# Kernel optimization log

Measured on AMD Instinct MI355X. Metric: run time of the kernel, lower is better.

The kernel has to match this reference:

```python
import jax, jax.numpy as jnp
import numpy as np

V, E, HS, HD = 32000, 64, 128, 128
S, T = 128, 48


def gru_cell(x, h, Wih, Whh, bih, bhh):
    # torch nn.GRU cell: gates stacked as [r, z, n]
    gi = x @ Wih.T + bih
    gh = h @ Whh.T + bhh
    ir, iz, inn = jnp.split(gi, 3, axis=-1)
    hr, hz, hn = jnp.split(gh, 3, axis=-1)
    r = jax.nn.sigmoid(ir + hr)
    z = jax.nn.sigmoid(iz + hz)
    n = jnp.tanh(inn + r * hn)
    return (1.0 - z) * n + z * h


def setup_inputs() -> dict:
    key = jax.random.key(0)
    ks = jax.random.split(key, 16)
    sc = 0.05
    inp = {
        'document': jax.random.randint(ks[0], (S, T), 0, V, dtype=jnp.int64),
        'enc_emb': jax.random.normal(ks[1], (V, E), jnp.float32) * sc,
        'enc_Wih': jax.random.normal(ks[2], (3 * HS, E), jnp.float32) * sc,
        'enc_Whh': jax.random.normal(ks[3], (3 * HS, HS), jnp.float32) * sc,
        'enc_bih': jax.random.normal(ks[4], (3 * HS,), jnp.float32) * sc,
        'enc_bhh': jax.random.normal(ks[5], (3 * HS,), jnp.float32) * sc,
        'doc_Wih': jax.random.normal(ks[6], (3 * HD, HS), jnp.float32) * sc,
        'doc_Whh': jax.random.normal(ks[7], (3 * HD, HD), jnp.float32) * sc,
        'doc_bih': jax.random.normal(ks[8], (3 * HD,), jnp.float32) * sc,
        'doc_bhh': jax.random.normal(ks[9], (3 * HD,), jnp.float32) * sc,
        'dec_emb': jax.random.normal(ks[10], (V, E), jnp.float32) * sc,
        'dec_Wih': jax.random.normal(ks[11], (3 * HS, E + HD), jnp.float32) * sc,
        'dec_Whh': jax.random.normal(ks[12], (3 * HS, HS), jnp.float32) * sc,
        'dec_bih': jax.random.normal(ks[13], (3 * HS,), jnp.float32) * sc,
        'dec_bhh': jax.random.normal(ks[14], (3 * HS,), jnp.float32) * sc,
        'fc_W': jax.random.normal(ks[15], (V, HS), jnp.float32) * sc,
        'fc_b': jnp.zeros((V,), jnp.float32),
    }
    return inp


def reference(document, enc_emb, enc_Wih, enc_Whh, enc_bih, enc_bhh,
              doc_Wih, doc_Whh, doc_bih, doc_bhh,
              dec_emb, dec_Wih, dec_Whh, dec_bih, dec_bhh, fc_W, fc_b):
    s, t = document.shape
    # --- sentence encoder: GRU over tokens, batch = sentences ---
    x = enc_emb[document]                       # [S, T, E]
    def enc_step(h, xt):
        return gru_cell(xt, h, enc_Wih, enc_Whh, enc_bih, enc_bhh), None
    h0 = jnp.zeros((s, HS), enc_emb.dtype)
    sent_vec, _ = jax.lax.scan(enc_step, h0, jnp.swapaxes(x, 0, 1))  # [S, HS]
    # --- document encoder: GRU over sentence vectors, batch = 1 ---
    def doc_step(h, sv):
        return gru_cell(sv[None, :], h, doc_Wih, doc_Whh, doc_bih, doc_bhh), None
    hd0 = jnp.zeros((1, HD), enc_emb.dtype)
    doc_h, _ = jax.lax.scan(doc_step, hd0, sent_vec)
    doc_vec = doc_h[0]                          # [HD]
    # --- teacher-forced decoder, vectorized over sentences ---
    dec_in = dec_emb[document[:, :-1]]          # [S, T-1, E]
    ctx = jnp.broadcast_to(doc_vec, (s, t - 1, HD))
    xs = jnp.swapaxes(jnp.concatenate([dec_in, ctx], axis=-1), 0, 1)  # [T-1, S, E+HD]
    def dec_step(h, xt):
        h2 = gru_cell(xt, h, dec_Wih, dec_Whh, dec_bih, dec_bhh)
        logits = h2 @ fc_W.T + fc_b
        return h2, logits
    _, logits = jax.lax.scan(dec_step, sent_vec, xs)  # [T-1, S, V]
    targets = document[:, 1:].T                 # [T-1, S]
    logp = jax.nn.log_softmax(logits, axis=-1)
    ll = jnp.take_along_axis(logp, targets[..., None], axis=-1)[..., 0]
    # per-sentence mean over steps, then mean over sentences == global mean
    return -jnp.mean(ll)
```

## Files before the change

### kernel.cpp

```cpp
#include <hip/hip_runtime.h>

typedef unsigned short ushort_t;
typedef short bf16x8 __attribute__((ext_vector_type(8)));
typedef float f32x4 __attribute__((ext_vector_type(4)));
typedef unsigned int u32x4 __attribute__((ext_vector_type(4)));
typedef _Float16 half2t __attribute__((ext_vector_type(2)));

#define LOG2E 1.4426950408889634f
#define LN2   0.6931471805599453f

__device__ __forceinline__ float bf2f(ushort_t u) {
    union { unsigned int i; float f; } v; v.i = ((unsigned int)u) << 16; return v.f;
}
__device__ __forceinline__ ushort_t f2bf(float f) {
    union { float f; unsigned int i; } v; v.f = f;
    unsigned int u = v.i;
    unsigned int r = (u + 0x7FFFu + ((u >> 16) & 1u)) >> 16;
    return (ushort_t)r;
}
__device__ __forceinline__ float hsum4(f32x4 v) { return (v[0] + v[1]) + (v[2] + v[3]); }
__device__ __forceinline__ float frcp(float x) { return __builtin_amdgcn_rcpf(x); }
__device__ __forceinline__ float fsig(float x) { return frcp(1.f + __expf(-x)); }
__device__ __forceinline__ float ftanh(float x) { return 1.f - 2.f * frcp(1.f + __expf(2.f * x)); }
__device__ __forceinline__ int hpad(int e) { return e + ((e >> 4) << 2); }
__device__ __forceinline__ float dot2(unsigned int w, unsigned int h, float acc) {
    union { unsigned int u; half2t h2; } a, b;
    a.u = w; b.u = h;
    return __builtin_amdgcn_fdot2(a.h2, b.h2, acc, false);
}
__device__ __forceinline__ float dpp_xor1_add(float x) {
    int m = __builtin_amdgcn_update_dpp(0, __builtin_bit_cast(int, x), 0xB1, 0xF, 0xF, true);
    return x + __builtin_bit_cast(float, m);
}
__device__ __forceinline__ float dpp_xor2_add(float x) {
    int m = __builtin_amdgcn_update_dpp(0, __builtin_bit_cast(int, x), 0x4E, 0xF, 0xF, true);
    return x + __builtin_bit_cast(float, m);
}
__device__ __forceinline__ ushort_t f2h(float f) {
    union { _Float16 h; ushort_t s; } c; c.h = (_Float16)f; return c.s;
}

__global__ void k_prep(const float* __restrict__ encWih, const float* __restrict__ encWhh,
                       const float* __restrict__ decWhh, const float* __restrict__ docWhh,
                       ushort_t* __restrict__ wencih, ushort_t* __restrict__ wenchh,
                       ushort_t* __restrict__ wdechh, ushort_t* __restrict__ wdoc) {
    int i = blockIdx.x * blockDim.x + threadIdx.x;
    const float* src; ushort_t* dst; int off;
    if (i < 6144)       { src = encWih; dst = wencih; off = i; }
    else if (i < 18432) { src = encWhh; dst = wenchh; off = i - 6144; }
    else if (i < 30720) { src = decWhh; dst = wdechh; off = i - 18432; }
    else if (i < 43008) { src = docWhh; dst = wdoc;   off = i - 30720; }
    else return;
    f32x4 v = ((const f32x4*)src)[off];
    union { ushort_t u[4]; unsigned long long q; } p;
    p.u[0] = f2h(v[0]); p.u[1] = f2h(v[1]); p.u[2] = f2h(v[2]); p.u[3] = f2h(v[3]);
    ((unsigned long long*)dst)[off] = p.q;
}

__global__ __launch_bounds__(768, 1) void k_encoder(
    const int* __restrict__ doc, const float* __restrict__ emb,
    const ushort_t* __restrict__ wih16, const ushort_t* __restrict__ whh16,
    const float* __restrict__ bih, const float* __restrict__ bhh,
    float* __restrict__ sent) {
    int s = blockIdx.x, t = threadIdx.x;
    int half = t & 1, j = t >> 1;
    __shared__ unsigned int xpk[32], hpk_[64];
    __shared__ float gi[384], gh[384];
    __shared__ int toks[48];
    u32x4 wi[4], wh[8];
    const ushort_t* pih = wih16 + j * 64 + half * 32;
    const ushort_t* phh = whh16 + j * 128 + half * 64;
#pragma unroll
    for (int k = 0; k < 4; k++) wi[k] = *(const u32x4*)(pih + k * 8);
#pragma unroll
    for (int k = 0; k < 8; k++) wh[k] = *(const u32x4*)(phh + k * 8);
    float bi = bih[j], bh = bhh[j];
    if (t < 48) toks[t] = doc[s * 48 + t];
    if (t < 64) hpk_[t] = 0u;
    __syncthreads();
    if (t < 64) ((ushort_t*)xpk)[t] = f2h(emb[(size_t)toks[0] * 64 + t]);
    float h_own = 0.f;
    __syncthreads();
    const unsigned int* xb = xpk + half * 16;
    const unsigned int* hb = hpk_ + half * 32;
    for (int tt = 0; tt < 48; tt++) {
        float xnext = (t < 64 && tt + 1 < 48) ? emb[(size_t)toks[tt + 1] * 64 + t] : 0.f;
        float a0 = 0.f, a1 = 0.f, b0 = 0.f, b1 = 0.f;
#pragma unroll
        for (int k = 0; k < 4; k++) {
            u32x4 xv = *(const u32x4*)(xb + k * 4);
            a0 = dot2(wi[k][0], xv[0], a0); a1 = dot2(wi[k][1], xv[1], a1);
            a0 = dot2(wi[k][2], xv[2], a0); a1 = dot2(wi[k][3], xv[3], a1);
        }
#pragma unroll
        for (int k = 0; k < 8; k++) {
            u32x4 hv = *(const u32x4*)(hb + k * 4);
            b0 = dot2(wh[k][0], hv[0], b0); b1 = dot2(wh[k][1], hv[1], b1);
            b0 = dot2(wh[k][2], hv[2], b0); b1 = dot2(wh[k][3], hv[3], b1);
        }
        float a = dpp_xor1_add(a0 + a1), b = dpp_xor1_add(b0 + b1);
        if (half == 0) { gi[j] = a + bi; gh[j] = b + bh; }
        __syncthreads();
        if (t < 128) {
            float r = fsig(gi[t] + gh[t]);
            float z = fsig(gi[t + 128] + gh[t + 128]);
            float n = ftanh(gi[t + 256] + r * gh[t + 256]);
            h_own = (1.f - z) * n + z * h_own;
            ((ushort_t*)hpk_)[t] = f2h(h_own);
        }
        if (t < 64 && tt + 1 < 48) ((ushort_t*)xpk)[t] = f2h(xnext);
        __syncthreads();
    }
    if (t < 128) sent[s * 128 + t] = h_own;
}

__global__ void k_doc_gi(const float* __restrict__ sv, const float* __restrict__ Wih,
                         const float* __restrict__ bih, float* __restrict__ gidoc) {
    int i = blockIdx.x, j = threadIdx.x;
    __shared__ f32x4 v4[32];
    if (j < 128) ((float*)v4)[j] = sv[i * 128 + j];
    __syncthreads();
    f32x4 a0 = {0,0,0,0}, a1 = {0,0,0,0};
#pragma unroll
    for (int k = 0; k < 32; k += 2) {
        a0 += *(const f32x4*)(Wih + j * 128 + k * 4) * v4[k];
        a1 += *(const f32x4*)(Wih + j * 128 + (k + 1) * 4) * v4[k + 1];
    }
    gidoc[i * 384 + j] = bih[j] + hsum4(a0 + a1);
}

__global__ __launch_bounds__(512, 1) __attribute__((amdgpu_waves_per_eu(1, 2)))
void k_mid(
    const float* __restrict__ gidoc, const ushort_t* __restrict__ wdoc,
    const float* __restrict__ dbhh, float* __restrict__ dvec,
    const int* __restrict__ doc, const float* __restrict__ demb,
    const float* __restrict__ dWih, float* __restrict__ gidec,
    const float* __restrict__ fcW, ushort_t* __restrict__ fcWb,
    const float* __restrict__ fcb, float* __restrict__ fcbs) {
    int bid = blockIdx.x, t = threadIdx.x;

    if (bid == 0) {
        int q = t & 3, e = t >> 2;
        __shared__ unsigned int hpk[2][64];
        u32x4 wr4[4], wz4[4], wn4[4];
        const ushort_t* wbase = wdoc + e * 128 + q * 32;
#pragma unroll
        for (int k = 0; k < 4; k++) {
            wr4[k] = *(const u32x4*)(wbase + k * 8);
            wz4[k] = *(const u32x4*)(wbase + 128 * 128 + k * 8);
            wn4[k] = *(const u32x4*)(wbase + 256 * 128 + k * 8);
        }
        float biasr = dbhh[e], biasz = dbhh[128 + e], biasn = dbhh[256 + e];
        float cr = gidoc[e], cz = gidoc[128 + e], cn = gidoc[256 + e];
        if (t < 64) hpk[0][t] = 0u;
        float he = 0.f;
        __syncthreads();
        for (int i = 0; i < 128; i++) {
            float nr = 0.f, nz = 0.f, nn = 0.f;
            if (i + 1 < 128) {
                const float* g = gidoc + (i + 1) * 384;
                nr = g[e]; nz = g[128 + e]; nn = g[256 + e];
            }
            const unsigned int* hp = &hpk[i & 1][q * 16];
            u32x4 hv[4];
            hv[0] = *(const u32x4*)(hp);
            hv[1] = *(const u32x4*)(hp + 4);
            hv[2] = *(const u32x4*)(hp + 8);
            hv[3] = *(const u32x4*)(hp + 12);
            float ra0 = 0.f, ra1 = 0.f, za0 = 0.f, za1 = 0.f, na0 = 0.f, na1 = 0.f;
#pragma unroll
            for (int k = 0; k < 4; k++) {
                u32x4 h4 = hv[k];
                ra0 = dot2(wr4[k][0], h4[0], ra0); ra1 = dot2(wr4[k][1], h4[1], ra1);
                ra0 = dot2(wr4[k][2], h4[2], ra0); ra1 = dot2(wr4[k][3], h4[3], ra1);
                za0 = dot2(wz4[k][0], h4[0], za0); za1 = dot2(wz4[k][1], h4[1], za1);
                za0 = dot2(wz4[k][2], h4[2], za0); za1 = dot2(wz4[k][3], h4[3], za1);
                na0 = dot2(wn4[k][0], h4[0], na0); na1 = dot2(wn4[k][1], h4[1], na1);
                na0 = dot2(wn4[k][2], h4[2], na0); na1 = dot2(wn4[k][3], h4[3], na1);
            }
            float rp = ra0 + ra1, zp = za0 + za1, np = na0 + na1;
            rp = dpp_xor2_add(dpp_xor1_add(rp));
            zp = dpp_xor2_add(dpp_xor1_add(zp));
            np = dpp_xor2_add(dpp_xor1_add(np));
            float r = fsig(cr + rp + biasr);
            float z = fsig(cz + zp + biasz);
            float n = ftanh(cn + r * (np + biasn));
            he = (1.f - z) * n + z * he;
            if (q == 0) ((ushort_t*)&hpk[(i & 1) ^ 1][0])[e] = f2h(he);
            __syncthreads();
            cr = nr; cz = nz; cn = nn;
        }
        if (q == 0) dvec[e] = he;
        return;
    }

    if (bid <= 128) {
        int s = bid - 1;
        __shared__ float xs[80];
        __shared__ int toks[48];
        if (t < 47) toks[t] = doc[s * 48 + t];
        __syncthreads();
        if (t < 64) xs[hpad(t)] = demb[(size_t)toks[0] * 64 + t];
        __syncthreads();
        f32x4 wih[16];
        if (t < 384) {
#pragma unroll
            for (int k = 0; k < 16; k++) wih[k] = *(const f32x4*)(dWih + t * 192 + k * 4);
        }
        for (int tt = 0; tt < 47; tt++) {
            float xnext = (t < 64 && tt + 1 < 47) ? demb[(size_t)toks[tt + 1] * 64 + t] : 0.f;
            if (t < 384) {
                f32x4 a0 = {0,0,0,0}, a1 = {0,0,0,0};
#pragma unroll
                for (int k = 0; k < 16; k += 2) {
                    a0 += wih[k] * (*(const f32x4*)(xs + k * 4 + (k >> 2) * 4));
                    a1 += wih[k + 1] * (*(const f32x4*)(xs + (k + 1) * 4 + ((k + 1) >> 2) * 4));
                }
                gidec[(tt * 128 + s) * 384 + t] = hsum4(a0 + a1);
            }
            __syncthreads();
            if (t < 64 && tt + 1 < 47) xs[hpad(t)] = xnext;
            __syncthreads();
        }
        return;
    }

    int i = (bid - 129) * 512 + t;
    if (i < 1024000) {
        f32x4 v = ((const f32x4*)fcW)[i];
        union { ushort_t u[4]; unsigned long long qq; } p;
        p.u[0] = f2bf(v[0] * LOG2E); p.u[1] = f2bf(v[1] * LOG2E);
        p.u[2] = f2bf(v[2] * LOG2E); p.u[3] = f2bf(v[3] * LOG2E);
        ((unsigned long long*)fcWb)[i] = p.qq;
    } else if (i < 1024000 + 8000) {
        int k = i - 1024000;
        f32x4 b = ((const f32x4*)fcb)[k];
        ((f32x4*)fcbs)[k] = b * LOG2E;
    }
}

__global__ void k_gctx(const float* __restrict__ Wih, const float* __restrict__ bih,
                       const float* __restrict__ dvec, float* __restrict__ gctx) {
    int j = threadIdx.x;
    __shared__ f32x4 v4[32];
    if (j < 128) ((float*)v4)[j] = dvec[j];
    __syncthreads();
    f32x4 a0 = {0,0,0,0}, a1 = {0,0,0,0};
#pragma unroll
    for (int k = 0; k < 32; k += 2) {
        a0 += *(const f32x4*)(Wih + j * 192 + 64 + k * 4) * v4[k];
        a1 += *(const f32x4*)(Wih + j * 192 + 64 + (k + 1) * 4) * v4[k + 1];
    }
    gctx[j] = bih[j] + hsum4(a0 + a1);
}

__global__ __launch_bounds__(768, 1) void k_dec_seq(
    const float* __restrict__ gidec, const ushort_t* __restrict__ whh16,
    const float* __restrict__ bhh, const float* __restrict__ sent,
    const float* __restrict__ gctx, ushort_t* __restrict__ h2b) {
    int s = blockIdx.x, t = threadIdx.x, half = t & 1, j = t >> 1;
    __shared__ unsigned int hpk_[64];
    __shared__ float gi[384], gh[384];
    u32x4 wh[8];
    const ushort_t* phh = whh16 + j * 128 + half * 64;
#pragma unroll
    for (int k = 0; k < 8; k++) wh[k] = *(const u32x4*)(phh + k * 8);
    float bh = bhh[j];
    float g_me = gctx[j];
    float h_own = 0.f;
    if (t < 128) { h_own = sent[s * 128 + t]; ((ushort_t*)hpk_)[t] = f2h(h_own); }
    float gval = (half == 0) ? (gidec[s * 384 + j] + g_me) : 0.f;
    __syncthreads();
    const unsigned int* hb = hpk_ + half * 32;
    for (int i = 0; i < 47; i++) {
        float gnext = (half == 0 && i + 1 < 47) ? (gidec[((i + 1) * 128 + s) * 384 + j] + g_me) : 0.f;
        float b0 = 0.f, b1 = 0.f;
#pragma unroll
        for (int k = 0; k < 8; k++) {
            u32x4 hv = *(const u32x4*)(hb + k * 4);
            b0 = dot2(wh[k][0], hv[0], b0); b1 = dot2(wh[k][1], hv[1], b1);
            b0 = dot2(wh[k][2], hv[2], b0); b1 = dot2(wh[k][3], hv[3], b1);
        }
        float b = dpp_xor1_add(b0 + b1);
        if (half == 0) { gh[j] = b + bh; gi[j] = gval; }
        __syncthreads();
        if (t < 128) {
            float r = fsig(gi[t] + gh[t]);
            float z = fsig(gi[t + 128] + gh[t + 128]);
            float n = ftanh(gi[t + 256] + r * gh[t + 256]);
            h_own = (1.f - z) * n + z * h_own;
            ((ushort_t*)hpk_)[t] = f2h(h_own);
            h2b[(i * 128 + s) * 128 + t] = f2bf(h_own);
        }
        __syncthreads();
        gval = gnext;
    }
}

__global__ void k_tl(const int* __restrict__ doc, const ushort_t* __restrict__ h2b,
                     const ushort_t* __restrict__ wb, const float* __restrict__ fcb,
                     float* __restrict__ tl) {
    int r = blockIdx.x * 4 + (threadIdx.x >> 6);
    int lane = threadIdx.x & 63;
    int s = r & 127, t = r >> 7;
    int tok = doc[s * 48 + t + 1];
    const ushort_t* hp = h2b + r * 128;
    const ushort_t* wp = wb + tok * 128;
    float acc = bf2f(hp[lane]) * bf2f(wp[lane]) + bf2f(hp[lane + 64]) * bf2f(wp[lane + 64]);
#pragma unroll
    for (int m = 32; m >= 1; m >>= 1) acc += __shfl_xor(acc, m);
    if (lane == 0) tl[r] = acc * LN2 + fcb[tok];
}

#define LSE_VC 10
#define LSE_NC 3200
#define LSE_NPAIR 25
__global__ __launch_bounds__(512, 2) void k_lse(
    const ushort_t* __restrict__ h2b, const ushort_t* __restrict__ wb,
    const float* __restrict__ fcbs, float* __restrict__ parts) {
    int rb = blockIdx.x / LSE_VC;
    int vc = blockIdx.x % LSE_VC;
    int t = threadIdx.x;
    int wave = t >> 6, lane = t & 63;
    int rg = wave >> 1, cg = wave & 1;
    int q = lane >> 4, l15 = lane & 15;

    __shared__ __align__(16) char ldsB[65536];

    int row0 = rb * 128 + rg * 32;
    bf16x8 a[2][4];
    const ushort_t* ap = h2b + (size_t)(row0 + l15) * 128 + q * 8;
#pragma unroll
    for (int m = 0; m < 2; m++)
#pragma unroll
        for (int c = 0; c < 4; c++) a[m][c] = *(const bf16x8*)(ap + m * 2048 + c * 32);

    const char* wbB = (const char*)wb;
    int so = ((t >> 4) << 8) + (((t & 15) ^ ((t >> 4) & 15)) << 4);
    char* dst1 = ldsB + wave * 1024;

#define LSE_STAGE(buf, cb) do { \
    const char* g_ = wbB + (size_t)(cb) * 256 + so; \
    char* d_ = dst1 + (buf) * 16384; \
    __builtin_amdgcn_global_load_lds((const __attribute__((address_space(1))) unsigned int*)(g_), \
                                     (__attribute__((address_space(3))) unsigned int*)(d_), 16, 0, 0); \
    __builtin_amdgcn_global_load_lds((const __attribute__((address_space(1))) unsigned int*)(g_ + 8192), \
                                     (__attribute__((address_space(3))) unsigned int*)(d_ + 8192), 16, 0, 0); \
} while (0)

    int ra[2][4];
#pragma unroll
    for (int c2 = 0; c2 < 2; c2++)
#pragma unroll
        for (int c = 0; c < 4; c++)
            ra[c2][c] = (cg * 32 + c2 * 16 + l15) * 256 + (((q + 4 * c) ^ l15) << 4);

    int cb0 = vc * LSE_NC;
    f32x4 se[2] = {{0,0,0,0},{0,0,0,0}};

    LSE_STAGE(0, cb0);
    LSE_STAGE(1, cb0 + 64);
    __syncthreads();
    int cur = 0;
    for (int it = 0; it < LSE_NPAIR; ++it) {
        if (it + 1 < LSE_NPAIR) {
            LSE_STAGE(2 * (cur ^ 1),     cb0 + (2 * it + 2) * 64);
            LSE_STAGE(2 * (cur ^ 1) + 1, cb0 + (2 * it + 3) * 64);
        }
        int colg = cb0 + 2 * it * 64 + cg * 32 + l15;
        float bA0 = fcbs[colg],      bA1 = fcbs[colg + 16];
        float bB0 = fcbs[colg + 64], bB1 = fcbs[colg + 80];
#pragma unroll
        for (int half = 0; half < 2; half++) {
            const char* bb = ldsB + (size_t)(2 * cur + half) * 16384;
            float bs0 = half ? bB0 : bA0;
            float bs1 = half ? bB1 : bA1;
            f32x4 acc[2][2] = {{{0,0,0,0},{0,0,0,0}},{{0,0,0,0},{0,0,0,0}}};
#pragma unroll
            for (int c = 0; c < 4; c++) {
                bf16x8 b0 = *(const bf16x8*)(bb + ra[0][c]);
                bf16x8 b1 = *(const bf16x8*)(bb + ra[1][c]);
                acc[0][0] = __builtin_amdgcn_mfma_f32_16x16x32_bf16(a[0][c], b0, acc[0][0], 0, 0, 0);
                acc[1][0] = __builtin_amdgcn_mfma_f32_16x16x32_bf16(a[1][c], b0, acc[1][0], 0, 0, 0);
                acc[0][1] = __builtin_amdgcn_mfma_f32_16x16x32_bf16(a[0][c], b1, acc[0][1], 0, 0, 0);
                acc[1][1] = __builtin_amdgcn_mfma_f32_16x16x32_bf16(a[1][c], b1, acc[1][1], 0, 0, 0);
            }
#pragma unroll
            for (int m = 0; m < 2; m++) {
#pragma unroll
                for (int r = 0; r < 4; r++)
                    se[m][r] += __builtin_amdgcn_exp2f(acc[m][0][r] + bs0)
                              + __builtin_amdgcn_exp2f(acc[m][1][r] + bs1);
            }
        }
        __syncthreads();
        cur ^= 1;
    }

#pragma unroll
    for (int m = 0; m < 2; m++) {
        f32x4 v = se[m];
#pragma unroll
        for (int d = 1; d < 16; d <<= 1) {
            v[0] += __shfl_xor(v[0], d);
            v[1] += __shfl_xor(v[1], d);
            v[2] += __shfl_xor(v[2], d);
            v[3] += __shfl_xor(v[3], d);
        }
        if (l15 == 0) {
            float* p = parts + (size_t)(vc * 2 + cg) * 6016 + row0 + m * 16 + q * 4;
            p[0] = v[0]; p[1] = v[1]; p[2] = v[2]; p[3] = v[3];
        }
    }
}

__global__ void k_final1(const float* __restrict__ parts, const float* __restrict__ tl,
                         float* __restrict__ rowloss) {
    int r = blockIdx.x * 128 + threadIdx.x;
    float tot = 0.f;
#pragma unroll 4
    for (int c = 0; c < 20; c++) tot += parts[(size_t)c * 6016 + r];
    rowloss[r] = logf(tot) - tl[r];
}

__global__ void k_final2(const float* __restrict__ rowloss, float* __restrict__ out) {
    __shared__ float red[512];
    int tid = threadIdx.x;
    float acc = 0.f;
    for (int r = tid; r < 6016; r += 512) acc += rowloss[r];
    red[tid] = acc;
    __syncthreads();
    for (int s = 256; s > 0; s >>= 1) {
        if (tid < s) red[tid] += red[tid + s];
        __syncthreads();
    }
    if (tid == 0) out[0] = red[0] / 6016.f;
}

extern "C" void kernel_launch(void* const* d_in, const int* in_sizes, int n_in,
                              void* d_out, int out_size, void* d_ws, size_t ws_size,
                              hipStream_t stream) {
    const int* doc = (const int*)d_in[0];
    const float* enc_emb = (const float*)d_in[1];
    const float* enc_Wih = (const float*)d_in[2];
    const float* enc_Whh = (const float*)d_in[3];
    const float* enc_bih = (const float*)d_in[4];
    const float* enc_bhh = (const float*)d_in[5];
    const float* doc_Wih = (const float*)d_in[6];
    const float* doc_Whh = (const float*)d_in[7];
    const float* doc_bih = (const float*)d_in[8];
    const float* doc_bhh = (const float*)d_in[9];
    const float* dec_emb = (const float*)d_in[10];
    const float* dec_Wih = (const float*)d_in[11];
    const float* dec_Whh = (const float*)d_in[12];
    const float* dec_bih = (const float*)d_in[13];
    const float* dec_bhh = (const float*)d_in[14];
    const float* fc_W = (const float*)d_in[15];
    const float* fc_b = (const float*)d_in[16];

    char* ws = (char*)d_ws;
    ushort_t* fcWb   = (ushort_t*)(ws + 0);
    float* sent      = (float*)(ws + 8192000);
    float* dvec      = (float*)(ws + 8257536);
    float* gidoc     = (float*)(ws + 8258048);
    float* gidec     = (float*)(ws + 8456192);
    ushort_t* h2b    = (ushort_t*)(ws + 17696768);
    float* tl        = (float*)(ws + 19236864);
    float* parts     = (float*)(ws + 19260928);
    float* rowloss   = (float*)(ws + 19742208);
    ushort_t* wdoc   = (ushort_t*)(ws + 19766272);
    float* fcbs      = (float*)(ws + 19864576);
    float* gctx      = (float*)(ws + 19992576);
    ushort_t* wencih = (ushort_t*)(ws + 19994112);
    ushort_t* wenchh = (ushort_t*)(ws + 20043264);
    ushort_t* wdechh = (ushort_t*)(ws + 20141568);
    float* out = (float*)d_out;

    k_prep<<<168, 256, 0, stream>>>(enc_Wih, enc_Whh, dec_Whh, doc_Whh,
                                    wencih, wenchh, wdechh, wdoc);
    k_encoder<<<128, 768, 0, stream>>>(doc, enc_emb, wencih, wenchh, enc_bih, enc_bhh, sent);
    k_doc_gi<<<128, 384, 0, stream>>>(sent, doc_Wih, doc_bih, gidoc);
    k_mid<<<1 + 128 + 2016, 512, 0, stream>>>(gidoc, wdoc, doc_bhh, dvec,
                                              doc, dec_emb, dec_Wih, gidec,
                                              fc_W, fcWb, fc_b, fcbs);
    k_gctx<<<1, 384, 0, stream>>>(dec_Wih, dec_bih, dvec, gctx);
    k_dec_seq<<<128, 768, 0, stream>>>(gidec, wdechh, dec_bhh, sent, gctx, h2b);
    k_tl<<<1504, 256, 0, stream>>>(doc, h2b, fcWb, fc_b, tl);
    k_lse<<<47 * LSE_VC, 512, 0, stream>>>(h2b, fcWb, fcbs, parts);
    k_final1<<<47, 128, 0, stream>>>(parts, tl, rowloss);
    k_final2<<<1, 512, 0, stream>>>(rowloss, out);
}
```

Baseline: 231.1 us.

## Fold gctx into decoder kernel and split LSE vocab into finer chunks

```diff
diff --git a/kernel.cpp b/kernel.cpp
--- a/kernel.cpp
+++ b/kernel.cpp
@@ -239,38 +239,37 @@
     }
 }
 
-__global__ void k_gctx(const float* __restrict__ Wih, const float* __restrict__ bih,
-                       const float* __restrict__ dvec, float* __restrict__ gctx) {
-    int j = threadIdx.x;
-    __shared__ f32x4 v4[32];
-    if (j < 128) ((float*)v4)[j] = dvec[j];
-    __syncthreads();
-    f32x4 a0 = {0,0,0,0}, a1 = {0,0,0,0};
-#pragma unroll
-    for (int k = 0; k < 32; k += 2) {
-        a0 += *(const f32x4*)(Wih + j * 192 + 64 + k * 4) * v4[k];
-        a1 += *(const f32x4*)(Wih + j * 192 + 64 + (k + 1) * 4) * v4[k + 1];
-    }
-    gctx[j] = bih[j] + hsum4(a0 + a1);
-}
-
 __global__ __launch_bounds__(768, 1) void k_dec_seq(
     const float* __restrict__ gidec, const ushort_t* __restrict__ whh16,
     const float* __restrict__ bhh, const float* __restrict__ sent,
-    const float* __restrict__ gctx, ushort_t* __restrict__ h2b) {
+    const float* __restrict__ dWih, const float* __restrict__ dbih,
+    const float* __restrict__ dvec, ushort_t* __restrict__ h2b) {
     int s = blockIdx.x, t = threadIdx.x, half = t & 1, j = t >> 1;
     __shared__ unsigned int hpk_[64];
     __shared__ float gi[384], gh[384];
+    __shared__ float gctxs[384];
+    __shared__ f32x4 dv4[32];
     u32x4 wh[8];
     const ushort_t* phh = whh16 + j * 128 + half * 64;
 #pragma unroll
     for (int k = 0; k < 8; k++) wh[k] = *(const u32x4*)(phh + k * 8);
     float bh = bhh[j];
-    float g_me = gctx[j];
+    if (t < 128) ((float*)dv4)[t] = dvec[t];
+    __syncthreads();
+    if (t < 384) {
+        f32x4 c0 = {0,0,0,0}, c1 = {0,0,0,0};
+#pragma unroll
+        for (int k = 0; k < 32; k += 2) {
+            c0 += *(const f32x4*)(dWih + t * 192 + 64 + k * 4) * dv4[k];
+            c1 += *(const f32x4*)(dWih + t * 192 + 64 + (k + 1) * 4) * dv4[k + 1];
+        }
+        gctxs[t] = dbih[t] + hsum4(c0 + c1);
+    }
     float h_own = 0.f;
     if (t < 128) { h_own = sent[s * 128 + t]; ((ushort_t*)hpk_)[t] = f2h(h_own); }
+    __syncthreads();
+    float g_me = gctxs[j];
     float gval = (half == 0) ? (gidec[s * 384 + j] + g_me) : 0.f;
-    __syncthreads();
     const unsigned int* hb = hpk_ + half * 32;
     for (int i = 0; i < 47; i++) {
         float gnext = (half == 0 && i + 1 < 47) ? (gidec[((i + 1) * 128 + s) * 384 + j] + g_me) : 0.f;
@@ -312,10 +311,10 @@
     if (lane == 0) tl[r] = acc * LN2 + fcb[tok];
 }
 
-#define LSE_VC 10
-#define LSE_NC 3200
-#define LSE_NPAIR 25
-__global__ __launch_bounds__(512, 2) void k_lse(
+#define LSE_VC 20
+#define LSE_NC 1600
+#define LSE_NT 25
+__global__ __launch_bounds__(512, 8) void k_lse(
     const ushort_t* __restrict__ h2b, const ushort_t* __restrict__ wb,
     const float* __restrict__ fcbs, float* __restrict__ parts) {
     int rb = blockIdx.x / LSE_VC;
@@ -325,7 +324,7 @@
     int rg = wave >> 1, cg = wave & 1;
     int q = lane >> 4, l15 = lane & 15;
 
-    __shared__ __align__(16) char ldsB[65536];
+    __shared__ __align__(16) char ldsB[32768];
 
     int row0 = rb * 128 + rg * 32;
     bf16x8 a[2][4];
@@ -359,39 +358,29 @@
     f32x4 se[2] = {{0,0,0,0},{0,0,0,0}};
 
     LSE_STAGE(0, cb0);
-    LSE_STAGE(1, cb0 + 64);
     __syncthreads();
     int cur = 0;
-    for (int it = 0; it < LSE_NPAIR; ++it) {
-        if (it + 1 < LSE_NPAIR) {
-            LSE_STAGE(2 * (cur ^ 1),     cb0 + (2 * it + 2) * 64);
-            LSE_STAGE(2 * (cur ^ 1) + 1, cb0 + (2 * it + 3) * 64);
-        }
-        int colg = cb0 + 2 * it * 64 + cg * 32 + l15;
-        float bA0 = fcbs[colg],      bA1 = fcbs[colg + 16];
-        float bB0 = fcbs[colg + 64], bB1 = fcbs[colg + 80];
-#pragma unroll
-        for (int half = 0; half < 2; half++) {
-            const char* bb = ldsB + (size_t)(2 * cur + half) * 16384;
-            float bs0 = half ? bB0 : bA0;
-            float bs1 = half ? bB1 : bA1;
-            f32x4 acc[2][2] = {{{0,0,0,0},{0,0,0,0}},{{0,0,0,0},{0,0,0,0}}};
-#pragma unroll
-            for (int c = 0; c < 4; c++) {
-                bf16x8 b0 = *(const bf16x8*)(bb + ra[0][c]);
-                bf16x8 b1 = *(const bf16x8*)(bb + ra[1][c]);
-                acc[0][0] = __builtin_amdgcn_mfma_f32_16x16x32_bf16(a[0][c], b0, acc[0][0], 0, 0, 0);
-                acc[1][0] = __builtin_amdgcn_mfma_f32_16x16x32_bf16(a[1][c], b0, acc[1][0], 0, 0, 0);
-                acc[0][1] = __builtin_amdgcn_mfma_f32_16x16x32_bf16(a[0][c], b1, acc[0][1], 0, 0, 0);
-                acc[1][1] = __builtin_amdgcn_mfma_f32_16x16x32_bf16(a[1][c], b1, acc[1][1], 0, 0, 0);
-            }
-#pragma unroll
-            for (int m = 0; m < 2; m++) {
-#pragma unroll
-                for (int r = 0; r < 4; r++)
-                    se[m][r] += __builtin_amdgcn_exp2f(acc[m][0][r] + bs0)
-                              + __builtin_amdgcn_exp2f(acc[m][1][r] + bs1);
-            }
+    for (int tile = 0; tile < LSE_NT; ++tile) {
+        if (tile + 1 < LSE_NT) LSE_STAGE(cur ^ 1, cb0 + (tile + 1) * 64);
+        const char* bb = ldsB + (cur << 14);
+        int colg = cb0 + tile * 64 + cg * 32 + l15;
+        float bs0 = fcbs[colg], bs1 = fcbs[colg + 16];
+        f32x4 acc[2][2] = {{{0,0,0,0},{0,0,0,0}},{{0,0,0,0},{0,0,0,0}}};
+#pragma unroll
+        for (int c = 0; c < 4; c++) {
+            bf16x8 b0 = *(const bf16x8*)(bb + ra[0][c]);
+            bf16x8 b1 = *(const bf16x8*)(bb + ra[1][c]);
+            acc[0][0] = __builtin_amdgcn_mfma_f32_16x16x32_bf16(a[0][c], b0, acc[0][0], 0, 0, 0);
+            acc[1][0] = __builtin_amdgcn_mfma_f32_16x16x32_bf16(a[1][c], b0, acc[1][0], 0, 0, 0);
+            acc[0][1] = __builtin_amdgcn_mfma_f32_16x16x32_bf16(a[0][c], b1, acc[0][1], 0, 0, 0);
+            acc[1][1] = __builtin_amdgcn_mfma_f32_16x16x32_bf16(a[1][c], b1, acc[1][1], 0, 0, 0);
+        }
+#pragma unroll
+        for (int m = 0; m < 2; m++) {
+#pragma unroll
+            for (int r = 0; r < 4; r++)
+                se[m][r] += __builtin_amdgcn_exp2f(acc[m][0][r] + bs0)
+                          + __builtin_amdgcn_exp2f(acc[m][1][r] + bs1);
         }
         __syncthreads();
         cur ^= 1;
@@ -418,8 +407,8 @@
                          float* __restrict__ rowloss) {
     int r = blockIdx.x * 128 + threadIdx.x;
     float tot = 0.f;
-#pragma unroll 4
-    for (int c = 0; c < 20; c++) tot += parts[(size_t)c * 6016 + r];
+#pragma unroll 8
+    for (int c = 0; c < 40; c++) tot += parts[(size_t)c * 6016 + r];
     rowloss[r] = logf(tot) - tl[r];
 }
 
@@ -467,13 +456,12 @@
     ushort_t* h2b    = (ushort_t*)(ws + 17696768);
     float* tl        = (float*)(ws + 19236864);
     float* parts     = (float*)(ws + 19260928);
-    float* rowloss   = (float*)(ws + 19742208);
-    ushort_t* wdoc   = (ushort_t*)(ws + 19766272);
-    float* fcbs      = (float*)(ws + 19864576);
-    float* gctx      = (float*)(ws + 19992576);
-    ushort_t* wencih = (ushort_t*)(ws + 19994112);
-    ushort_t* wenchh = (ushort_t*)(ws + 20043264);
-    ushort_t* wdechh = (ushort_t*)(ws + 20141568);
+    float* rowloss   = (float*)(ws + 20223488);
+    ushort_t* wdoc   = (ushort_t*)(ws + 20247552);
+    float* fcbs      = (float*)(ws + 20345856);
+    ushort_t* wencih = (ushort_t*)(ws + 20473856);
+    ushort_t* wenchh = (ushort_t*)(ws + 20523008);
+    ushort_t* wdechh = (ushort_t*)(ws + 20621312);
     float* out = (float*)d_out;
 
     k_prep<<<168, 256, 0, stream>>>(enc_Wih, enc_Whh, dec_Whh, doc_Whh,
@@ -483,8 +471,8 @@
     k_mid<<<1 + 128 + 2016, 512, 0, stream>>>(gidoc, wdoc, doc_bhh, dvec,
                                               doc, dec_emb, dec_Wih, gidec,
                                               fc_W, fcWb, fc_b, fcbs);
-    k_gctx<<<1, 384, 0, stream>>>(dec_Wih, dec_bih, dvec, gctx);
-    k_dec_seq<<<128, 768, 0, stream>>>(gidec, wdechh, dec_bhh, sent, gctx, h2b);
+    k_dec_seq<<<128, 768, 0, stream>>>(gidec, wdechh, dec_bhh, sent,
+                                       dec_Wih, dec_bih, dvec, h2b);
     k_tl<<<1504, 256, 0, stream>>>(doc, h2b, fcWb, fc_b, tl);
     k_lse<<<47 * LSE_VC, 512, 0, stream>>>(h2b, fcWb, fcbs, parts);
     k_final1<<<47, 128, 0, stream>>>(parts, tl, rowloss);
```

Result: slower. 283.9 us (+22.8%).
